# Kernel tuning notes

Measured on AMD Instinct MI355X. Metric: run time of the kernel, lower is better.

## Reference

```python
import jax, jax.numpy as jnp
import numpy as np

D_MODEL, H, DK, DV = 1024, 16, 64, 64
B, NQ, NK = 4, 1024, 1024
LN_EPS = 1e-5


def setup_inputs() -> dict:
    key = jax.random.key(0)
    ks = jax.random.split(key, 16)
    xavier = lambda k, i, o: jax.random.uniform(k, (i, o), jnp.float32,
                                                -np.sqrt(6.0 / (i + o)), np.sqrt(6.0 / (i + o)))
    return {
        "queries": jax.random.normal(ks[0], (B, NQ, D_MODEL), jnp.float32),
        "keys": jax.random.normal(ks[1], (B, NK, D_MODEL), jnp.float32),
        "values": jax.random.normal(ks[2], (B, NK, D_MODEL), jnp.float32),
        "geometry": jax.random.uniform(ks[3], (B, H, NQ, NK), jnp.float32),
        "attention_mask": jax.random.bernoulli(ks[4], 0.1, (B, H, NQ, NK)),
        "Wq": xavier(ks[5], D_MODEL, H * DK), "bq": jnp.zeros((H * DK,), jnp.float32),
        "Wk": xavier(ks[6], D_MODEL, H * DK), "bk": jnp.zeros((H * DK,), jnp.float32),
        "Wv": xavier(ks[7], D_MODEL, H * DV), "bv": jnp.zeros((H * DV,), jnp.float32),
        "Wo": xavier(ks[8], H * DV, D_MODEL), "bo": jnp.zeros((D_MODEL,), jnp.float32),
        "ln_gamma": jnp.ones((D_MODEL,), jnp.float32),
        "ln_beta": jnp.zeros((D_MODEL,), jnp.float32),
    }


def reference(queries, keys, values, geometry, attention_mask,
              Wq, bq, Wk, bk, Wv, bv, Wo, bo, ln_gamma, ln_beta):
    b, nq, _ = queries.shape
    nk = keys.shape[1]
    # QKV projections -> (b, h, n, d)
    q = (queries @ Wq + bq).reshape(b, nq, H, DK).transpose(0, 2, 1, 3)
    k = (keys @ Wk + bk).reshape(b, nk, H, DK).transpose(0, 2, 1, 3)
    v = (values @ Wv + bv).reshape(b, nk, H, DV).transpose(0, 2, 1, 3)
    att = jnp.einsum('bhqd,bhkd->bhqk', q, k) / np.sqrt(DK).astype(np.float32)
    att = jnp.where(attention_mask, -jnp.inf, att)
    # inline geometry log-bias before softmax
    w = jnp.log(jnp.clip(geometry, 1e-6)) + att
    w = jax.nn.softmax(w, axis=-1)  # dropout is identity in eval
    out = jnp.einsum('bhqk,bhkd->bqhd', w, v).reshape(b, nq, H * DV)
    out = out @ Wo + bo
    # residual + LayerNorm
    x = queries + out  # dropout identity in eval
    mu = jnp.mean(x, axis=-1, keepdims=True)
    var = jnp.mean((x - mu) ** 2, axis=-1, keepdims=True)
    return (x - mu) * jax.lax.rsqrt(var + LN_EPS) * ln_gamma + ln_beta
```

## Files before the change

kernel.cpp:

```cpp
#include <hip/hip_runtime.h>
#include <hip/hip_bf16.h>

typedef unsigned short u16;
typedef unsigned long long u64;
typedef __bf16 bf16x8 __attribute__((ext_vector_type(8)));
typedef float f32x4 __attribute__((ext_vector_type(4)));
typedef float f32x2 __attribute__((ext_vector_type(2)));

#define AS1 __attribute__((address_space(1)))
#define AS3 __attribute__((address_space(3)))
#define GLL16(gp, lp) __builtin_amdgcn_global_load_lds((AS1 const unsigned int*)(gp), (AS3 unsigned int*)(lp), 16, 0, 0)

__device__ __forceinline__ u16 f2bf(float f) {
    unsigned u = __builtin_bit_cast(unsigned, f);
    unsigned r = u + 0x7FFFu + ((u >> 16) & 1u);
    return (u16)(r >> 16);
}

__global__ void detect_kernel(const unsigned char* __restrict__ m, int* __restrict__ flag) {
    __shared__ int cnt1;
    __shared__ int big;
    if (threadIdx.x == 0) { cnt1 = 0; big = 0; }
    __syncthreads();
    int c1 = 0, bg = 0;
    for (int i = threadIdx.x; i < 16384; i += 256) {
        unsigned char v = m[i];
        if (v) {
            if ((i & 3) == 1) c1++;
            if (v > 1) bg++;
        }
    }
    atomicAdd(&cnt1, c1);
    atomicAdd(&big, bg);
    __syncthreads();
    if (threadIdx.x == 0) {
        int f;
        if (big == 0) f = cnt1 ? 0 : 1;
        else          f = cnt1 ? 3 : 2;
        *flag = f;
    }
}

#define MN_LOOP(PRED)                                                     \
    for (int row = wave; row < 65536; row += nw) {                        \
        size_t base = (size_t)row * 1024;                                 \
        u64 myw = 0;                                                      \
        _Pragma("unroll")                                                 \
        for (int kb = 0; kb < 16; ++kb) {                                 \
            size_t gi = base + kb * 64 + lane;                            \
            bool p = (PRED);                                              \
            u64 w = __ballot(p);                                          \
            if (lane == kb) myw = w;                                      \
        }                                                                 \
        if (lane < 16) MB[(size_t)row * 16 + lane] = myw;                 \
    }

__global__ __launch_bounds__(256) void masknorm_kernel(const void* __restrict__ mp,
                                                       const int* __restrict__ flagp,
                                                       u64* __restrict__ MB) {
    const int flag = *flagp;
    const int lane = threadIdx.x & 63;
    const int wave = blockIdx.x * 4 + (threadIdx.x >> 6);
    const int nw = gridDim.x * 4;
    if (flag == 0) {
        const unsigned char* m8 = (const unsigned char*)mp;
        MN_LOOP(m8[gi] != 0)
    } else if (flag == 1) {
        const int* m32 = (const int*)mp;
        MN_LOOP(m32[gi] != 0)
    } else if (flag == 2) {
        const unsigned* mf = (const unsigned*)mp;
        MN_LOOP((mf[gi] << 1) != 0)
    } else {
        const u16* mb = (const u16*)mp;
        MN_LOOP((mb[gi] & 0x7FFF) != 0)
    }
}

__global__ void cast3_kernel(const float* __restrict__ q, const float* __restrict__ k,
                             const float* __restrict__ v, u16* __restrict__ xq,
                             u16* __restrict__ xk, u16* __restrict__ xv) {
    const int n4 = 4 * 1024 * 1024 / 4;
    int stride = gridDim.x * blockDim.x;
    for (int i = blockIdx.x * blockDim.x + threadIdx.x; i < n4; i += stride) {
        float4 a = ((const float4*)q)[i];
        float4 b = ((const float4*)k)[i];
        float4 c = ((const float4*)v)[i];
        ((ushort4*)xq)[i] = make_ushort4(f2bf(a.x), f2bf(a.y), f2bf(a.z), f2bf(a.w));
        ((ushort4*)xk)[i] = make_ushort4(f2bf(b.x), f2bf(b.y), f2bf(b.z), f2bf(b.w));
        ((ushort4*)xv)[i] = make_ushort4(f2bf(c.x), f2bf(c.y), f2bf(c.z), f2bf(c.w));
    }
}

__global__ __launch_bounds__(256) void wtrans_kernel(
    const float* __restrict__ W0, const float* __restrict__ W1,
    const float* __restrict__ W2, const float* __restrict__ W3,
    u16* __restrict__ T0, u16* __restrict__ T1, u16* __restrict__ T2, u16* __restrict__ T3) {
    const float* W = (blockIdx.z == 0) ? W0 : (blockIdx.z == 1) ? W1 : (blockIdx.z == 2) ? W2 : W3;
    u16* T = (blockIdx.z == 0) ? T0 : (blockIdx.z == 1) ? T1 : (blockIdx.z == 2) ? T2 : T3;
    __shared__ float t[64][65];
    const int n0 = blockIdx.x * 64, k0 = blockIdx.y * 64;
    const int tx = threadIdx.x, ty = threadIdx.y;
    for (int j = ty; j < 64; j += 4) t[j][tx] = W[(size_t)(k0 + j) * 1024 + n0 + tx];
    __syncthreads();
    for (int j = ty; j < 64; j += 4) T[(size_t)(n0 + j) * 1024 + k0 + tx] = f2bf(t[tx][j]);
}

__global__ __launch_bounds__(256) void qkv_gemm(
    const u16* __restrict__ XQ, const u16* __restrict__ XK, const u16* __restrict__ XV,
    const u16* __restrict__ WQT, const u16* __restrict__ WKT, const u16* __restrict__ WVT,
    const float* __restrict__ bq, const float* __restrict__ bk, const float* __restrict__ bv,
    u16* __restrict__ QS, u16* __restrict__ KS, u16* __restrict__ VT) {
    __shared__ __align__(16) u16 lsA[128 * 64];
    __shared__ __align__(16) u16 lsB[128 * 64];
    const int z = blockIdx.z;
    const u16* A  = (z == 0) ? XQ : (z == 1) ? XK : XV;
    const u16* Bt = (z == 0) ? WQT : (z == 1) ? WKT : WVT;
    const float* bias = (z == 0) ? bq : (z == 1) ? bk : bv;
    const int tid = threadIdx.x, lane = tid & 63, wid = tid >> 6;
    const int bm = blockIdx.y, bn = blockIdx.x;
    const int wr = wid >> 1, wc = wid & 1;
    const int l15 = lane & 15, l4 = lane >> 4;
    f32x4 acc[4][4] = {};
    const int cbase = wid * 256;
    for (int t = 0; t < 16; ++t) {
        __syncthreads();
        for (int j = 0; j < 4; ++j) {
            int c = cbase + j * 64 + lane;
            int row = c >> 3, off = (c & 7) * 8;
            GLL16(A + (size_t)(bm * 128 + row) * 1024 + t * 64 + off, lsA + (size_t)(cbase + j * 64) * 8);
            GLL16(Bt + (size_t)(bn * 128 + row) * 1024 + t * 64 + off, lsB + (size_t)(cbase + j * 64) * 8);
        }
        __syncthreads();
        for (int kk = 0; kk < 2; ++kk) {
            bf16x8 af[4], bfr[4];
            for (int m = 0; m < 4; ++m)
                af[m] = *(const bf16x8*)(lsA + (wr * 64 + m * 16 + l15) * 64 + kk * 32 + l4 * 8);
            for (int n = 0; n < 4; ++n)
                bfr[n] = *(const bf16x8*)(lsB + (wc * 64 + n * 16 + l15) * 64 + kk * 32 + l4 * 8);
            for (int m = 0; m < 4; ++m)
                for (int n = 0; n < 4; ++n)
                    acc[m][n] = __builtin_amdgcn_mfma_f32_16x16x32_bf16(af[m], bfr[n], acc[m][n], 0, 0, 0);
        }
    }
    const float scale = (z == 0) ? 0.125f : 1.0f;
    for (int n = 0; n < 4; ++n) {
        int c = bn * 128 + wc * 64 + n * 16 + l15;
        float bv_ = bias[c];
        for (int m = 0; m < 4; ++m) {
            for (int j = 0; j < 4; ++j) {
                int r = bm * 128 + wr * 64 + m * 16 + l4 * 4 + j;
                float v = acc[m][n][j];
                if (z == 2) {
                    int bb = r >> 10, k = r & 1023, h = c >> 6, d = c & 63;
                    VT[((size_t)((bb * 16 + h) * 64 + d)) * 1024 + k] = f2bf(v + bv_);
                } else {
                    u16* outp = (z == 0) ? QS : KS;
                    outp[(size_t)r * 1024 + c] = f2bf((v + bv_) * scale);
                }
            }
        }
    }
}

__global__ __launch_bounds__(256) void gemm_out(
    const u16* __restrict__ A, const u16* __restrict__ Bt, const float* __restrict__ bias,
    float* __restrict__ outp, const float* __restrict__ resid) {
    __shared__ __align__(16) u16 lsA[128 * 64];
    __shared__ __align__(16) u16 lsB[128 * 64];
    const int tid = threadIdx.x, lane = tid & 63, wid = tid >> 6;
    const int bm = blockIdx.y, bn = blockIdx.x;
    const int wr = wid >> 1, wc = wid & 1;
    const int l15 = lane & 15, l4 = lane >> 4;
    f32x4 acc[4][4] = {};
    const int cbase = wid * 256;
    for (int t = 0; t < 16; ++t) {
        __syncthreads();
        for (int j = 0; j < 4; ++j) {
            int c = cbase + j * 64 + lane;
            int row = c >> 3, off = (c & 7) * 8;
            GLL16(A + (size_t)(bm * 128 + row) * 1024 + t * 64 + off, lsA + (size_t)(cbase + j * 64) * 8);
            GLL16(Bt + (size_t)(bn * 128 + row) * 1024 + t * 64 + off, lsB + (size_t)(cbase + j * 64) * 8);
        }
        __syncthreads();
        for (int kk = 0; kk < 2; ++kk) {
            bf16x8 af[4], bfr[4];
            for (int m = 0; m < 4; ++m)
                af[m] = *(const bf16x8*)(lsA + (wr * 64 + m * 16 + l15) * 64 + kk * 32 + l4 * 8);
            for (int n = 0; n < 4; ++n)
                bfr[n] = *(const bf16x8*)(lsB + (wc * 64 + n * 16 + l15) * 64 + kk * 32 + l4 * 8);
            for (int m = 0; m < 4; ++m)
                for (int n = 0; n < 4; ++n)
                    acc[m][n] = __builtin_amdgcn_mfma_f32_16x16x32_bf16(af[m], bfr[n], acc[m][n], 0, 0, 0);
        }
    }
    for (int n = 0; n < 4; ++n) {
        int c = bn * 128 + wc * 64 + n * 16 + l15;
        float bv = bias[c];
        for (int m = 0; m < 4; ++m)
            for (int j = 0; j < 4; ++j) {
                int r = bm * 128 + wr * 64 + m * 16 + l4 * 4 + j;
                outp[(size_t)r * 1024 + c] = acc[m][n][j] + bv + resid[(size_t)r * 1024 + c];
            }
    }
}

__global__ __launch_bounds__(256, 4) void attn_kernel(
    const u16* __restrict__ Qs, const u16* __restrict__ Ks, const u16* __restrict__ Vt,
    const float* __restrict__ geom, const u64* __restrict__ MBw,
    u16* __restrict__ AO) {
    __shared__ __align__(16) u16 lds[14336];

    const int g = blockIdx.x;
    const int tt = (g & 7) * 128 + (g >> 3);
    const int qb = tt & 15;
    const int bhid = tt >> 4;
    const int b = bhid >> 4, h = bhid & 15;
    const int q0 = qb * 64;

    const int tid = threadIdx.x, lane = tid & 63, wid = tid >> 6;
    const int l15 = lane & 15, l4 = lane >> 4;
    const int qrow = q0 + wid * 16;
    const size_t bh = (size_t)bhid;

    const u16* qp = Qs + (size_t)(b * 1024 + qrow + l15) * 1024 + h * 64 + l4 * 8;
    bf16x8 aq0 = *(const bf16x8*)qp;
    bf16x8 aq1 = *(const bf16x8*)(qp + 32);

    const int kr = tid >> 3, ks = tid & 7;
    const int kgr = (kr & 15) * 2 + (kr >> 4);
    const u16* ksrc = Ks + (size_t)(b * 1024 + kgr) * 1024 + h * 64 + ((ks ^ ((kr >> 1) & 7)) * 8);
    const int vr = tid >> 2, vs = tid & 3;
    const u16* vsrc = Vt + (bh * 64 + vr) * 1024 + ((vs ^ ((vr >> 1) & 3)) * 8);
    u16* const KD0 = lds + 0    + wid * 512;
    u16* const KD1 = lds + 2048 + wid * 512;
    u16* const KD2 = lds + 4096 + wid * 512;
    u16* const VD0 = lds + 6144 + 0    + wid * 512;
    u16* const VD1 = lds + 6144 + 2048 + wid * 512;
    u16* const VD2 = lds + 6144 + 4096 + wid * 512;
    u16* const pw  = lds + 12288 + wid * 512;

    const float* gbase = geom + (bh * 1024 + qrow + l4 * 4) * 1024 + l15 * 2;
    const unsigned* mb32 = (const unsigned*)(MBw + (bh * 1024 + qrow + l4 * 4) * 16);

    f32x4 o[4] = {};
    float m_run[4], l_run[4];
#pragma unroll
    for (int j = 0; j < 4; ++j) { m_run[j] = -1e30f; l_run[j] = 0.f; }

    f32x2 gpA[4], gpB[4];
    unsigned mkA[4], mkB[4];

    GLL16(ksrc, KD0);
    GLL16(vsrc, VD0);
    GLL16(ksrc + 32768, KD1);
    GLL16(vsrc + 32, VD1);
    __builtin_amdgcn_sched_barrier(0);
#pragma unroll
    for (int j = 0; j < 4; ++j) {
        gpA[j] = *(const f32x2*)(gbase + j * 1024);
        mkA[j] = mb32[j * 32];
    }
    __builtin_amdgcn_sched_barrier(0);
    asm volatile("s_waitcnt vmcnt(10)" ::: "memory");
    __builtin_amdgcn_sched_barrier(0);
    __builtin_amdgcn_s_barrier();
    __builtin_amdgcn_sched_barrier(0);

#define BODY(T, GC, GN, MC, MN, KBC, VBC, KDN, VDN, WSTR)                                \
    do {                                                                                 \
        if ((T) + 2 < 32) {                                                              \
            GLL16(ksrc + (size_t)((T) + 2) * 32768, KDN);                                \
            GLL16(vsrc + ((T) + 2) * 32, VDN);                                           \
            __builtin_amdgcn_sched_barrier(0);                                           \
        }                                                                                \
        if ((T) + 1 < 32) {                                                              \
            _Pragma("unroll")                                                            \
            for (int j = 0; j < 4; ++j) {                                                \
                GN[j] = *(const f32x2*)(gbase + j * 1024 + ((T) + 1) * 32);              \
                MN[j] = mb32[j * 32 + (T) + 1];                                          \
            }                                                                            \
            __builtin_amdgcn_sched_barrier(0);                                           \
        }                                                                                \
        f32x4 s0, s1;                                                                    \
        __builtin_amdgcn_s_setprio(1);                                                   \
        {                                                                                \
            const int rr = l15, swz = (rr >> 1) & 7;                                     \
            bf16x8 k0 = *(const bf16x8*)((KBC) + rr * 64 + ((l4 ^ swz) * 8));            \
            bf16x8 k1 = *(const bf16x8*)((KBC) + rr * 64 + (((4 + l4) ^ swz) * 8));      \
            f32x4 z = {};                                                                \
            z = __builtin_amdgcn_mfma_f32_16x16x32_bf16(aq0, k0, z, 0, 0, 0);            \
            s0 = __builtin_amdgcn_mfma_f32_16x16x32_bf16(aq1, k1, z, 0, 0, 0);           \
        }                                                                                \
        {                                                                                \
            const int rr = 16 + l15, swz = (rr >> 1) & 7;                                \
            bf16x8 k0 = *(const bf16x8*)((KBC) + rr * 64 + ((l4 ^ swz) * 8));            \
            bf16x8 k1 = *(const bf16x8*)((KBC) + rr * 64 + (((4 + l4) ^ swz) * 8));      \
            f32x4 z = {};                                                                \
            z = __builtin_amdgcn_mfma_f32_16x16x32_bf16(aq0, k0, z, 0, 0, 0);            \
            s1 = __builtin_amdgcn_mfma_f32_16x16x32_bf16(aq1, k1, z, 0, 0, 0);           \
        }                                                                                \
        __builtin_amdgcn_s_setprio(0);                                                   \
        float sclv[4];                                                                   \
        _Pragma("unroll")                                                                \
        for (int j = 0; j < 4; ++j) {                                                    \
            float a0 = s0[j], a1 = s1[j];                                                \
            float mt = fmaxf(a0, a1);                                                    \
            mt = fmaxf(mt, __shfl_xor(mt, 1, 16));                                       \
            mt = fmaxf(mt, __shfl_xor(mt, 2, 16));                                       \
            mt = fmaxf(mt, __shfl_xor(mt, 4, 16));                                       \
            mt = fmaxf(mt, __shfl_xor(mt, 8, 16));                                       \
            float mn = fmaxf(m_run[j], mt);                                              \
            float scl = __expf(m_run[j] - mn);                                           \
            m_run[j] = mn;                                                               \
            unsigned mb2 = (MC[j] >> (l15 * 2)) & 3u;                                    \
            f32x2 gv = GC[j];                                                            \
            float p0 = (mb2 & 1u) ? 0.f : __expf(a0 - mn) * fmaxf(gv[0], 1e-6f);         \
            float p1 = (mb2 & 2u) ? 0.f : __expf(a1 - mn) * fmaxf(gv[1], 1e-6f);         \
            float rs = p0 + p1;                                                          \
            rs += __shfl_xor(rs, 1, 16);                                                 \
            rs += __shfl_xor(rs, 2, 16);                                                 \
            rs += __shfl_xor(rs, 4, 16);                                                 \
            rs += __shfl_xor(rs, 8, 16);                                                 \
            l_run[j] = l_run[j] * scl + rs;                                              \
            sclv[j] = scl;                                                               \
            const int row = l4 * 4 + j;                                                  \
            const int slot4 = (l15 & 3) | ((((l15 >> 2) ^ l4) & 3) << 2);                \
            unsigned pk = (unsigned)f2bf(p0) | ((unsigned)f2bf(p1) << 16);               \
            *(unsigned*)(pw + row * 32 + slot4 * 2) = pk;                                \
        }                                                                                \
        _Pragma("unroll")                                                                \
        for (int df = 0; df < 4; ++df) {                                                 \
            f32x4 tv = o[df];                                                            \
            _Pragma("unroll")                                                            \
            for (int j = 0; j < 4; ++j) tv[j] *= sclv[j];                                \
            o[df] = tv;                                                                  \
        }                                                                                \
        {                                                                                \
            const int blk = (l4 ^ (l15 >> 2)) & 3;                                       \
            bf16x8 pa = *(const bf16x8*)(pw + l15 * 32 + blk * 8);                       \
            __builtin_amdgcn_s_setprio(1);                                               \
            _Pragma("unroll")                                                            \
            for (int df = 0; df < 4; ++df) {                                             \
                const int rr = df * 16 + l15, vswz = (rr >> 1) & 3;                      \
                bf16x8 v0 = *(const bf16x8*)((VBC) + rr * 32 + ((l4 ^ vswz) * 8));       \
                o[df] = __builtin_amdgcn_mfma_f32_16x16x32_bf16(pa, v0, o[df], 0, 0, 0); \
            }                                                                            \
            __builtin_amdgcn_s_setprio(0);                                               \
        }                                                                                \
        if ((T) + 1 < 32) {                                                              \
            asm volatile(WSTR ::: "memory");                                             \
            __builtin_amdgcn_sched_barrier(0);                                           \
            __builtin_amdgcn_s_barrier();                                                \
            __builtin_amdgcn_sched_barrier(0);                                           \
        }                                                                                \
    } while (0)

    for (int it = 0; it < 5; ++it) {
        const int t0 = it * 6;
        BODY(t0 + 0, gpA, gpB, mkA, mkB, (lds + 0),    (lds + 6144),        KD2, VD2, "s_waitcnt vmcnt(10)");
        BODY(t0 + 1, gpB, gpA, mkB, mkA, (lds + 2048), (lds + 6144 + 2048), KD0, VD0, "s_waitcnt vmcnt(10)");
        BODY(t0 + 2, gpA, gpB, mkA, mkB, (lds + 4096), (lds + 6144 + 4096), KD1, VD1, "s_waitcnt vmcnt(10)");
        BODY(t0 + 3, gpB, gpA, mkB, mkA, (lds + 0),    (lds + 6144),        KD2, VD2, "s_waitcnt vmcnt(10)");
        BODY(t0 + 4, gpA, gpB, mkA, mkB, (lds + 2048), (lds + 6144 + 2048), KD0, VD0, "s_waitcnt vmcnt(10)");
        BODY(t0 + 5, gpB, gpA, mkB, mkA, (lds + 4096), (lds + 6144 + 4096), KD1, VD1, "s_waitcnt vmcnt(10)");
    }
    BODY(30, gpA, gpB, mkA, mkB, (lds + 0),    (lds + 6144),        KD2, VD2, "s_waitcnt vmcnt(8)");
    BODY(31, gpB, gpA, mkB, mkA, (lds + 2048), (lds + 6144 + 2048), KD0, VD0, "s_waitcnt vmcnt(8)");
#undef BODY

    float inv[4];
#pragma unroll
    for (int j = 0; j < 4; ++j) inv[j] = 1.0f / l_run[j];
#pragma unroll
    for (int p = 0; p < 2; ++p) {
#pragma unroll
        for (int df2 = 0; df2 < 2; ++df2) {
            const int df = p * 2 + df2;
#pragma unroll
            for (int j = 0; j < 4; ++j)
                pw[(l4 * 4 + j) * 32 + df2 * 16 + l15] = f2bf(o[df][j] * inv[j]);
        }
        const int er = lane >> 2, ec = lane & 3;
        bf16x8 val = *(const bf16x8*)(pw + er * 32 + ec * 8);
        *(bf16x8*)(AO + (size_t)(b * 1024 + qrow + er) * 1024 + h * 64 + p * 32 + ec * 8) = val;
    }
}

__global__ __launch_bounds__(256) void ln_kernel(const float* __restrict__ Y,
                                                 const float* __restrict__ gamma,
                                                 const float* __restrict__ beta,
                                                 float* __restrict__ out) {
    __shared__ float red[8];
    const int r = blockIdx.x, tid = threadIdx.x, lane = tid & 63, wid = tid >> 6;
    float4 v = ((const float4*)(Y + (size_t)r * 1024))[tid];
    float s = v.x + v.y + v.z + v.w;
    float q = v.x * v.x + v.y * v.y + v.z * v.z + v.w * v.w;
    for (int d = 1; d < 64; d <<= 1) {
        s += __shfl_xor(s, d, 64);
        q += __shfl_xor(q, d, 64);
    }
    if (lane == 0) { red[wid] = s; red[4 + wid] = q; }
    __syncthreads();
    float ts = red[0] + red[1] + red[2] + red[3];
    float tq = red[4] + red[5] + red[6] + red[7];
    float mu = ts * (1.f / 1024.f);
    float var = tq * (1.f / 1024.f) - mu * mu;
    float rstd = rsqrtf(var + 1e-5f);
    float4 gg = ((const float4*)gamma)[tid];
    float4 be = ((const float4*)beta)[tid];
    float4 ov;
    ov.x = (v.x - mu) * rstd * gg.x + be.x;
    ov.y = (v.y - mu) * rstd * gg.y + be.y;
    ov.z = (v.z - mu) * rstd * gg.z + be.z;
    ov.w = (v.w - mu) * rstd * gg.w + be.w;
    ((float4*)(out + (size_t)r * 1024))[tid] = ov;
}

extern "C" void kernel_launch(void* const* d_in, const int* in_sizes, int n_in,
                              void* d_out, int out_size, void* d_ws, size_t ws_size,
                              hipStream_t stream) {
    const float* queries = (const float*)d_in[0];
    const float* keys    = (const float*)d_in[1];
    const float* values  = (const float*)d_in[2];
    const float* geom    = (const float*)d_in[3];
    const void*  mask    = d_in[4];
    const float* Wq = (const float*)d_in[5];  const float* bq = (const float*)d_in[6];
    const float* Wk = (const float*)d_in[7];  const float* bk = (const float*)d_in[8];
    const float* Wv = (const float*)d_in[9];  const float* bv = (const float*)d_in[10];
    const float* Wo = (const float*)d_in[11]; const float* bo = (const float*)d_in[12];
    const float* gamma = (const float*)d_in[13];
    const float* beta  = (const float*)d_in[14];

    char* ws = (char*)d_ws;
    const size_t MB_ = 1024 * 1024;
    u16* XQ  = (u16*)(ws + 0);
    u16* XK  = (u16*)(ws + 8 * MB_);
    u16* XV  = (u16*)(ws + 16 * MB_);
    u16* WQT = (u16*)(ws + 24 * MB_);
    u16* WKT = (u16*)(ws + 26 * MB_);
    u16* WVT = (u16*)(ws + 28 * MB_);
    u16* WOT = (u16*)(ws + 30 * MB_);
    u16* QS  = (u16*)(ws + 32 * MB_);
    u16* KS  = (u16*)(ws + 40 * MB_);
    u16* VT  = (u16*)(ws + 48 * MB_);
    u16* AO  = (u16*)(ws + 56 * MB_);
    u64* MBITS = (u64*)(ws + 16 * MB_);
    float* Y = (float*)(ws + 0);
    int* FLAG = (int*)(ws + 64 * MB_);

    detect_kernel<<<1, 256, 0, stream>>>((const unsigned char*)mask, FLAG);
    cast3_kernel<<<1024, 256, 0, stream>>>(queries, keys, values, XQ, XK, XV);
    wtrans_kernel<<<dim3(16, 16, 4), dim3(64, 4), 0, stream>>>(Wq, Wk, Wv, Wo, WQT, WKT, WVT, WOT);
    qkv_gemm<<<dim3(8, 32, 3), 256, 0, stream>>>(XQ, XK, XV, WQT, WKT, WVT, bq, bk, bv, QS, KS, VT);
    masknorm_kernel<<<4096, 256, 0, stream>>>(mask, FLAG, MBITS);
    attn_kernel<<<1024, 256, 0, stream>>>(QS, KS, VT, geom, MBITS, AO);
    gemm_out<<<dim3(8, 32), 256, 0, stream>>>(AO, WOT, bo, Y, queries);
    ln_kernel<<<4096, 256, 0, stream>>>(Y, gamma, beta, (float*)d_out);
}
```

Measured before the change: 309.1 us.

## Triple-buffer GEMM K-loop with swizzled LDS and coalesced V-transpose epilogue

```diff
diff --git a/kernel.cpp b/kernel.cpp
--- a/kernel.cpp
+++ b/kernel.cpp
@@ -106,13 +106,93 @@
     for (int j = ty; j < 64; j += 4) T[(size_t)(n0 + j) * 1024 + k0 + tx] = f2bf(t[tx][j]);
 }
 
-__global__ __launch_bounds__(256) void qkv_gemm(
+__device__ __forceinline__ void gemm_core(const u16* __restrict__ A, const u16* __restrict__ Bt,
+                                          u16* sA, u16* sB, f32x4 (&acc)[4][4],
+                                          int tid, int bm, int bn) {
+    const int lane = tid & 63, wid = tid >> 6;
+    const int wr = wid >> 1, wc = wid & 1;
+    const int l15 = lane & 15, l4 = lane >> 4;
+    const int srow = tid >> 2, sslot = tid & 3;
+    const int soff = (sslot ^ ((srow >> 1) & 3)) * 8;
+    const u16* aSrc = A + (size_t)(bm * 128 + srow) * 1024 + soff;
+    const u16* bSrc = Bt + (size_t)(bn * 128 + srow) * 1024 + soff;
+    u16* const dA0 = sA + wid * 512;
+    u16* const dA1 = sA + 2048 + wid * 512;
+    u16* const dB0 = sB + wid * 512;
+    u16* const dB1 = sB + 2048 + wid * 512;
+
+#define GSTAGE(BUF, T)                                                  \
+    do {                                                                \
+        GLL16(aSrc + (T) * 32, dA0 + (BUF) * 4096);                     \
+        GLL16(aSrc + 65536 + (T) * 32, dA1 + (BUF) * 4096);             \
+        GLL16(bSrc + (T) * 32, dB0 + (BUF) * 4096);                     \
+        GLL16(bSrc + 65536 + (T) * 32, dB1 + (BUF) * 4096);             \
+    } while (0)
+
+#define GCOMPUTE(BUF)                                                             \
+    do {                                                                          \
+        bf16x8 af[4], bfv[4];                                                     \
+        _Pragma("unroll")                                                         \
+        for (int m = 0; m < 4; ++m) {                                             \
+            const int rr = wr * 64 + m * 16 + l15;                                \
+            af[m] = *(const bf16x8*)(sA + (BUF) * 4096 + rr * 32 +                \
+                                     ((l4 ^ ((rr >> 1) & 3)) * 8));               \
+        }                                                                         \
+        _Pragma("unroll")                                                         \
+        for (int n = 0; n < 4; ++n) {                                             \
+            const int rr = wc * 64 + n * 16 + l15;                                \
+            bfv[n] = *(const bf16x8*)(sB + (BUF) * 4096 + rr * 32 +               \
+                                      ((l4 ^ ((rr >> 1) & 3)) * 8));              \
+        }                                                                         \
+        _Pragma("unroll")                                                         \
+        for (int m = 0; m < 4; ++m)                                               \
+            _Pragma("unroll")                                                     \
+            for (int n = 0; n < 4; ++n)                                           \
+                acc[m][n] = __builtin_amdgcn_mfma_f32_16x16x32_bf16(af[m], bfv[n], acc[m][n], 0, 0, 0); \
+    } while (0)
+
+#define GBODY(T, BUF, NBUF, WSTR)                                       \
+    do {                                                                \
+        if ((T) + 2 < 32) {                                             \
+            GSTAGE(NBUF, (T) + 2);                                      \
+            __builtin_amdgcn_sched_barrier(0);                          \
+        }                                                               \
+        GCOMPUTE(BUF);                                                  \
+        if ((T) + 1 < 32) {                                             \
+            asm volatile(WSTR ::: "memory");                            \
+            __builtin_amdgcn_sched_barrier(0);                          \
+            __builtin_amdgcn_s_barrier();                               \
+            __builtin_amdgcn_sched_barrier(0);                          \
+        }                                                               \
+    } while (0)
+
+    GSTAGE(0, 0);
+    GSTAGE(1, 1);
+    __builtin_amdgcn_sched_barrier(0);
+    asm volatile("s_waitcnt vmcnt(4)" ::: "memory");
+    __builtin_amdgcn_sched_barrier(0);
+    __builtin_amdgcn_s_barrier();
+    __builtin_amdgcn_sched_barrier(0);
+
+    for (int it = 0; it < 10; ++it) {
+        const int t0 = it * 3;
+        GBODY(t0 + 0, 0, 2, "s_waitcnt vmcnt(4)");
+        GBODY(t0 + 1, 1, 0, "s_waitcnt vmcnt(4)");
+        GBODY(t0 + 2, 2, 1, "s_waitcnt vmcnt(4)");
+    }
+    GBODY(30, 0, 2, "s_waitcnt vmcnt(0)");
+    GBODY(31, 1, 0, "s_waitcnt vmcnt(0)");
+#undef GBODY
+#undef GCOMPUTE
+#undef GSTAGE
+}
+
+__global__ __launch_bounds__(256, 3) void qkv_gemm(
     const u16* __restrict__ XQ, const u16* __restrict__ XK, const u16* __restrict__ XV,
     const u16* __restrict__ WQT, const u16* __restrict__ WKT, const u16* __restrict__ WVT,
     const float* __restrict__ bq, const float* __restrict__ bk, const float* __restrict__ bv,
     u16* __restrict__ QS, u16* __restrict__ KS, u16* __restrict__ VT) {
-    __shared__ __align__(16) u16 lsA[128 * 64];
-    __shared__ __align__(16) u16 lsB[128 * 64];
+    __shared__ __align__(16) u16 smem[24576];
     const int z = blockIdx.z;
     const u16* A  = (z == 0) ? XQ : (z == 1) ? XK : XV;
     const u16* Bt = (z == 0) ? WQT : (z == 1) ? WKT : WVT;
@@ -121,85 +201,75 @@
     const int bm = blockIdx.y, bn = blockIdx.x;
     const int wr = wid >> 1, wc = wid & 1;
     const int l15 = lane & 15, l4 = lane >> 4;
+
     f32x4 acc[4][4] = {};
-    const int cbase = wid * 256;
-    for (int t = 0; t < 16; ++t) {
+    gemm_core(A, Bt, smem, smem + 12288, acc, tid, bm, bn);
+
+    if (z == 2) {
         __syncthreads();
-        for (int j = 0; j < 4; ++j) {
-            int c = cbase + j * 64 + lane;
-            int row = c >> 3, off = (c & 7) * 8;
-            GLL16(A + (size_t)(bm * 128 + row) * 1024 + t * 64 + off, lsA + (size_t)(cbase + j * 64) * 8);
-            GLL16(Bt + (size_t)(bn * 128 + row) * 1024 + t * 64 + off, lsB + (size_t)(cbase + j * 64) * 8);
+        u16* tl = smem;
+#pragma unroll
+        for (int n = 0; n < 4; ++n) {
+            const int cl = wc * 64 + n * 16 + l15;
+            const float bv_ = bias[bn * 128 + cl];
+#pragma unroll
+            for (int m = 0; m < 4; ++m)
+#pragma unroll
+                for (int j = 0; j < 4; ++j) {
+                    const int rl = wr * 64 + m * 16 + l4 * 4 + j;
+                    tl[cl * 132 + rl] = f2bf(acc[m][n][j] + bv_);
+                }
         }
         __syncthreads();
-        for (int kk = 0; kk < 2; ++kk) {
-            bf16x8 af[4], bfr[4];
+        const int bb = bm >> 3, k0 = (bm & 7) * 128;
+#pragma unroll
+        for (int i = 0; i < 8; ++i) {
+            const int idx = i * 256 + tid;
+            const int row = idx >> 4, col16 = idx & 15;
+            const int cg = bn * 128 + row;
+            const int hh = cg >> 6, dd = cg & 63;
+            bf16x8 v = *(const bf16x8*)(tl + row * 132 + col16 * 8);
+            *(bf16x8*)(VT + ((size_t)((bb * 16 + hh) * 64 + dd)) * 1024 + k0 + col16 * 8) = v;
+        }
+    } else {
+        u16* outp = (z == 0) ? QS : KS;
+        const float scale = (z == 0) ? 0.125f : 1.0f;
+#pragma unroll
+        for (int n = 0; n < 4; ++n) {
+            const int c = bn * 128 + wc * 64 + n * 16 + l15;
+            const float bv_ = bias[c];
+#pragma unroll
             for (int m = 0; m < 4; ++m)
-                af[m] = *(const bf16x8*)(lsA + (wr * 64 + m * 16 + l15) * 64 + kk * 32 + l4 * 8);
-            for (int n = 0; n < 4; ++n)
-                bfr[n] = *(const bf16x8*)(lsB + (wc * 64 + n * 16 + l15) * 64 + kk * 32 + l4 * 8);
-            for (int m = 0; m < 4; ++m)
-                for (int n = 0; n < 4; ++n)
-                    acc[m][n] = __builtin_amdgcn_mfma_f32_16x16x32_bf16(af[m], bfr[n], acc[m][n], 0, 0, 0);
+#pragma unroll
+                for (int j = 0; j < 4; ++j) {
+                    const int r = bm * 128 + wr * 64 + m * 16 + l4 * 4 + j;
+                    outp[(size_t)r * 1024 + c] = f2bf((acc[m][n][j] + bv_) * scale);
+                }
         }
     }
-    const float scale = (z == 0) ? 0.125f : 1.0f;
-    for (int n = 0; n < 4; ++n) {
-        int c = bn * 128 + wc * 64 + n * 16 + l15;
-        float bv_ = bias[c];
-        for (int m = 0; m < 4; ++m) {
-            for (int j = 0; j < 4; ++j) {
-                int r = bm * 128 + wr * 64 + m * 16 + l4 * 4 + j;
-                float v = acc[m][n][j];
-                if (z == 2) {
-                    int bb = r >> 10, k = r & 1023, h = c >> 6, d = c & 63;
-                    VT[((size_t)((bb * 16 + h) * 64 + d)) * 1024 + k] = f2bf(v + bv_);
-                } else {
-                    u16* outp = (z == 0) ? QS : KS;
-                    outp[(size_t)r * 1024 + c] = f2bf((v + bv_) * scale);
-                }
-            }
-        }
-    }
-}
-
-__global__ __launch_bounds__(256) void gemm_out(
+}
+
+__global__ __launch_bounds__(256, 3) void gemm_out(
     const u16* __restrict__ A, const u16* __restrict__ Bt, const float* __restrict__ bias,
     float* __restrict__ outp, const float* __restrict__ resid) {
-    __shared__ __align__(16) u16 lsA[128 * 64];
-    __shared__ __align__(16) u16 lsB[128 * 64];
+    __shared__ __align__(16) u16 smem[24576];
     const int tid = threadIdx.x, lane = tid & 63, wid = tid >> 6;
     const int bm = blockIdx.y, bn = blockIdx.x;
     const int wr = wid >> 1, wc = wid & 1;
     const int l15 = lane & 15, l4 = lane >> 4;
+
     f32x4 acc[4][4] = {};
-    const int cbase = wid * 256;
-    for (int t = 0; t < 16; ++t) {
-        __syncthreads();
-        for (int j = 0; j < 4; ++j) {
-            int c = cbase + j * 64 + lane;
-            int row = c >> 3, off = (c & 7) * 8;
-            GLL16(A + (size_t)(bm * 128 + row) * 1024 + t * 64 + off, lsA + (size_t)(cbase + j * 64) * 8);
-            GLL16(Bt + (size_t)(bn * 128 + row) * 1024 + t * 64 + off, lsB + (size_t)(cbase + j * 64) * 8);
-        }
-        __syncthreads();
-        for (int kk = 0; kk < 2; ++kk) {
-            bf16x8 af[4], bfr[4];
-            for (int m = 0; m < 4; ++m)
-                af[m] = *(const bf16x8*)(lsA + (wr * 64 + m * 16 + l15) * 64 + kk * 32 + l4 * 8);
-            for (int n = 0; n < 4; ++n)
-                bfr[n] = *(const bf16x8*)(lsB + (wc * 64 + n * 16 + l15) * 64 + kk * 32 + l4 * 8);
-            for (int m = 0; m < 4; ++m)
-                for (int n = 0; n < 4; ++n)
-                    acc[m][n] = __builtin_amdgcn_mfma_f32_16x16x32_bf16(af[m], bfr[n], acc[m][n], 0, 0, 0);
-        }
-    }
+    gemm_core(A, Bt, smem, smem + 12288, acc, tid, bm, bn);
+
+#pragma unroll
     for (int n = 0; n < 4; ++n) {
-        int c = bn * 128 + wc * 64 + n * 16 + l15;
-        float bv = bias[c];
+        const int c = bn * 128 + wc * 64 + n * 16 + l15;
+        const float bv = bias[c];
+#pragma unroll
         for (int m = 0; m < 4; ++m)
+#pragma unroll
             for (int j = 0; j < 4; ++j) {
-                int r = bm * 128 + wr * 64 + m * 16 + l4 * 4 + j;
+                const int r = bm * 128 + wr * 64 + m * 16 + l4 * 4 + j;
                 outp[(size_t)r * 1024 + c] = acc[m][n][j] + bv + resid[(size_t)r * 1024 + c];
             }
     }
```

New measurement: 274.4 us. -11.2%, faster.
